# Kernel optimization log

Measured on AMD Instinct MI355X. Metric: run time of the kernel, lower is better.

The kernel has to match this reference:

```python
import jax, jax.numpy as jnp
import numpy as np

K = 3            # kernel size (odd)
CO, CI = 16, 16  # out/in channels

def setup_inputs() -> dict:
    key = jax.random.key(0)
    k1, k2, k3, k4 = jax.random.split(key, 4)
    B, C, H, W = 4, CI, 128, 128
    input_data = jax.random.normal(k1, (B, C, H, W), dtype=jnp.float32)
    # fixation coordinates in pixel units
    foa_xy = jax.random.uniform(k2, (B, 2), dtype=jnp.float32) * jnp.array([W, H], jnp.float32)
    hidden = 256
    W1 = jax.random.normal(k3, (2, hidden), dtype=jnp.float32) * (1.0 / jnp.sqrt(2.0))
    b1 = jnp.zeros((hidden,), jnp.float32)
    W2 = jax.random.normal(k4, (hidden, CO * CI * K * K), dtype=jnp.float32) * (1.0 / jnp.sqrt(hidden))
    b2 = jnp.zeros((CO * CI * K * K,), jnp.float32)
    return {"input_data": input_data, "foa_xy": foa_xy, "W1": W1, "b1": b1, "W2": W2, "b2": b2}

def _unfold_reflect(x, k):
    # x: [B, C, H, W] -> patches [B, C, k*k, H*W], reflect padding, stride 1, dilation 1
    B, C, H, W = x.shape
    pad = (k - 1) // 2
    xp = jnp.pad(x, ((0, 0), (0, 0), (pad, pad), (pad, pad)), mode="reflect")
    rows = [xp[:, :, i:i + H, j:j + W] for i in range(k) for j in range(k)]
    return jnp.stack(rows, axis=2).reshape(B, C, k * k, H * W)

def reference(input_data, foa_xy, W1, b1, W2, b2):
    B, C, H, W = input_data.shape
    # coordinate grid [H*W, 2] as (x, y), matching torch meshgrid(ij) + stack(xx, yy)
    ys = jnp.arange(H, dtype=jnp.float32)
    xs = jnp.arange(W, dtype=jnp.float32)
    yy, xx = jnp.meshgrid(ys, xs, indexing="ij")
    coords = jnp.stack([xx.ravel(), yy.ravel()], axis=1)         # [HW, 2]
    net_in = (coords[None, :, :] - foa_xy[:, None, :]).reshape(B * H * W, 2)
    # kernel-generating MLP
    h = jax.nn.relu(net_in @ W1 + b1)
    net_out = h @ W2 + b2                                        # [B*HW, CO*CI*K*K]
    kernel = net_out.reshape(B, H * W, CO, CI, K * K)            # [B, P, o, i, q]
    patches = _unfold_reflect(input_data, K)                     # [B, CI, K*K, HW]
    # per-pixel conv: sum over in-channels and kernel taps
    out = jnp.einsum("biqp,bpoiq->bop", patches, kernel)         # [B, CO, HW]
    return out.reshape(B, CO, H, W)
```

## Files before the change

kernel.cpp:

```cpp
#include <hip/hip_runtime.h>

#define CI    16
#define CO    16
#define HID   256
#define KPAD  288
#define NKK   9
#define NKH   8
#define NCH   144
#define IMGH  128
#define IMGW  128
#define NMS   8
#define RSTR  132
#define RLEN  130
#define KKSTR (NCH * 32)
#define OSTRS (NKK * NCH * 32)
#define MGOFF (4 * NKH * 512)

typedef float f32x4  __attribute__((ext_vector_type(4)));
typedef float f32x2  __attribute__((ext_vector_type(2)));
typedef short bf16x8 __attribute__((ext_vector_type(8)));

__device__ __host__ __forceinline__ short f2bf(float f) {
  union { float f; unsigned u; } c; c.f = f;
  unsigned b = c.u + 0x7FFFu + ((c.u >> 16) & 1u);
  return (short)(b >> 16);
}

__global__ void prep_w2(const float* __restrict__ W2, const float* __restrict__ b2,
                        short* __restrict__ W2b) {
  __shared__ float tile[32][65];
  const int kk = blockIdx.x % NKK;
  const int colbase = (blockIdx.x / NKK) * 64;
  const int tid = threadIdx.x;

  for (int e = tid; e < 2048; e += 256) {
    int klr = e >> 6;
    int cc  = e & 63;
    int col = colbase + cc;
    float v;
    if (kk < 8) v = W2[(kk * 32 + klr) * (CO * NCH) + col];
    else        v = (klr == 0) ? b2[col] : 0.f;
    tile[klr][cc] = v;
  }
  __syncthreads();
  for (int e = tid; e < 2048; e += 256) {
    int cc = e >> 5;
    int kl = e & 31;
    int col = colbase + cc;
    int o = col / NCH;
    int n = col - o * NCH;
    int i = n / 9, q = n - i * 9;
    int dyr = q / 3, dx = q - dyr * 3;
    int np = dx * 48 + i * 3 + dyr;
    W2b[(((o * NKK + kk) * NCH + np) << 5) + kl] = f2bf(tile[kl][cc]);
  }
}

__global__ __launch_bounds__(512, 4)
void ngconv_main(const float* __restrict__ in, const float* __restrict__ foa,
                 const float* __restrict__ W1, const float* __restrict__ b1,
                 const short* __restrict__ W2b, float* __restrict__ out) {
  __shared__ short shHf[64 * 512];
  __shared__ short shPatch[48 * RSTR];

  const int tid  = threadIdx.x;
  const int lane = tid & 63;
  const int wv8  = tid >> 6;
  const int mg   = wv8 >> 2;
  const int wo   = wv8 & 3;
  const int c15  = lane & 15;
  const int quad = lane >> 4;

  const int blk = blockIdx.x;
  const int b   = blk >> 7;
  const int y   = blk & 127;

  const float fx  = foa[b * 2 + 0];
  const float fy  = foa[b * 2 + 1];
  const float dyv = (float)y - fy;

  const int ry0 = (y == 0) ? 1 : (y - 1);
  const int ry2 = (y == IMGH - 1) ? (IMGH - 2) : (y + 1);

  for (int e = tid; e < 48 * RLEN; e += 512) {
    int r  = e / RLEN;
    int xx = e - r * RLEN;
    int i = r / 3, dyr = r - i * 3;
    int ryr = (dyr == 0) ? ry0 : ((dyr == 1) ? y : ry2);
    int x = xx - 1;
    x = (x < 0) ? 1 : ((x > IMGW - 1) ? (IMGW - 2) : x);
    shPatch[r * RSTR + xx] = f2bf(in[((b * CI + i) * IMGH + ryr) * IMGW + x]);
  }

  for (int g = tid; g < 128 * 32; g += 512) {
    int px = g & 127;
    int ks = g >> 7;
    int k0 = ks << 3;
    float dxv = (float)px - fx;
    short hv[8];
    #pragma unroll
    for (int j = 0; j < 8; ++j) {
      int k = k0 + j;
      float h = fmaxf(fmaf(dxv, W1[k], fmaf(dyv, W1[HID + k], b1[k])), 0.f);
      hv[j] = f2bf(h);
    }
    int ms = px >> 4;
    int kk = k0 >> 5;
    int lslot = ((k0 & 31) >> 3) * 16 + (px & 15);
    *(bf16x8*)&shHf[((ms * NKH + kk) << 9) + (lslot << 3)] = *(bf16x8*)hv;
  }

  bf16x8 af8 = (bf16x8){0, 0, 0, 0, 0, 0, 0, 0};
  if (quad == 0) af8[0] = (short)0x3F80;

  __syncthreads();

  const short* shHg = shHf + mg * MGOFF;

  #pragma unroll 1
  for (int oj = 0; oj < 4; ++oj) {
    const int o = wo + oj * 4;
    const short* Bo = W2b + o * OSTRS + (c15 << 5) + (quad << 3);

    f32x2 P2[8];
    #pragma unroll
    for (int t = 0; t < 8; ++t) P2[t] = (f32x2){0.f, 0.f};

    #pragma unroll 1
    for (int pass = 0; pass < 3; ++pass) {
      const short* Bp = Bo + (pass * 3) * 512;
      f32x4 acc[4][3];
      #pragma unroll
      for (int ms = 0; ms < 4; ++ms)
        #pragma unroll
        for (int j = 0; j < 3; ++j)
          acc[ms][j] = (f32x4){0.f, 0.f, 0.f, 0.f};

      bf16x8 bE[3], bO[3];
      #pragma unroll
      for (int j = 0; j < 3; ++j) bE[j] = *(const bf16x8*)&Bp[j << 9];

      #pragma unroll 1
      for (int t = 0; t < 4; ++t) {
        const int kkE = 2 * t;
        #pragma unroll
        for (int j = 0; j < 3; ++j)
          bO[j] = *(const bf16x8*)&Bp[(kkE + 1) * KKSTR + (j << 9)];
        {
          const short* hp = shHg + (kkE << 9) + (lane << 3);
          #pragma unroll
          for (int ms = 0; ms < 4; ++ms) {
            bf16x8 af = *(const bf16x8*)&hp[ms * (NKH << 9)];
            #pragma unroll
            for (int j = 0; j < 3; ++j)
              acc[ms][j] = __builtin_amdgcn_mfma_f32_16x16x32_bf16(
                  af, bE[j], acc[ms][j], 0, 0, 0);
          }
        }
        #pragma unroll
        for (int j = 0; j < 3; ++j)
          bE[j] = *(const bf16x8*)&Bp[(kkE + 2) * KKSTR + (j << 9)];
        {
          const short* hp = shHg + ((kkE + 1) << 9) + (lane << 3);
          #pragma unroll
          for (int ms = 0; ms < 4; ++ms) {
            bf16x8 af = *(const bf16x8*)&hp[ms * (NKH << 9)];
            #pragma unroll
            for (int j = 0; j < 3; ++j)
              acc[ms][j] = __builtin_amdgcn_mfma_f32_16x16x32_bf16(
                  af, bO[j], acc[ms][j], 0, 0, 0);
          }
        }
      }
      {
        #pragma unroll
        for (int ms = 0; ms < 4; ++ms)
          #pragma unroll
          for (int j = 0; j < 3; ++j)
            acc[ms][j] = __builtin_amdgcn_mfma_f32_16x16x32_bf16(
                af8, bE[j], acc[ms][j], 0, 0, 0);
      }

      const int sh = pass << 4;
      #pragma unroll
      for (int j = 0; j < 3; ++j) {
        const short* prow = &shPatch[((j << 4) + c15) * RSTR + (mg << 6) + (quad << 2)];
        #pragma unroll
        for (int ms = 0; ms < 4; ++ms) {
          uint2 u0 = *(const uint2*)&prow[ms * 16];
          unsigned u1 = *(const unsigned*)&prow[ms * 16 + 4];
          unsigned long long a0 =
              (unsigned long long)u0.x | ((unsigned long long)u0.y << 32);
          unsigned long long a1 =
              (unsigned long long)u0.y | ((unsigned long long)u1 << 32);
          unsigned d0 = (unsigned)(a0 >> sh);
          unsigned d1 = (unsigned)(a1 >> sh);
          float p0 = __uint_as_float(d0 << 16);
          float p1 = __uint_as_float(d0 & 0xFFFF0000u);
          float p2 = __uint_as_float(d1 << 16);
          float p3 = __uint_as_float(d1 & 0xFFFF0000u);
          f32x2 a01 = {acc[ms][j][0], acc[ms][j][1]};
          f32x2 a23 = {acc[ms][j][2], acc[ms][j][3]};
          P2[ms * 2 + 0] += a01 * (f32x2){p0, p1};
          P2[ms * 2 + 1] += a23 * (f32x2){p2, p3};
        }
      }
    }

    float P[16];
    #pragma unroll
    for (int t = 0; t < 16; ++t) P[t] = P2[t >> 1][t & 1];
    #pragma unroll
    for (int m = 8; m >= 1; m >>= 1) {
      const bool hi = (c15 & m) != 0;
      #pragma unroll
      for (int j = 0; j < m; ++j) {
        float keep = hi ? P[j + m] : P[j];
        float send = hi ? P[j] : P[j + m];
        float recv = __shfl_xor(send, m, 64);
        P[j] = keep + recv;
      }
    }

    const int x = (mg << 6) + (c15 >> 2) * 16 + quad * 4 + (c15 & 3);
    out[((b * CO + o) * IMGH + y) * IMGW + x] = P[0];
  }
}

extern "C" void kernel_launch(void* const* d_in, const int* in_sizes, int n_in,
                              void* d_out, int out_size, void* d_ws, size_t ws_size,
                              hipStream_t stream) {
  const float* in  = (const float*)d_in[0];
  const float* foa = (const float*)d_in[1];
  const float* W1  = (const float*)d_in[2];
  const float* b1  = (const float*)d_in[3];
  const float* W2  = (const float*)d_in[4];
  const float* b2  = (const float*)d_in[5];
  float* out = (float*)d_out;
  short* W2b = (short*)d_ws;

  prep_w2<<<324, 256, 0, stream>>>(W2, b2, W2b);
  ngconv_main<<<512, 512, 0, stream>>>(in, foa, W1, b1, W2b, out);
}
```

Baseline: 188.1 us.

## Halve block to 4 waves, compute two output channels per wave, stage stores in LDS

Shrinks the block from 8 to 4 waves. Each wave now accumulates two output channels at once, so every hidden-activation LDS fragment feeds twice as many MFMAs. Output rows are staged in shared memory and written as coalesced float2 stores instead of scattered per-lane stores. The cost is doubled accumulator registers (96 floats of acc plus 32 partial sums), fewer waves per block, and extra block-level barriers per channel pair.

```diff
diff --git a/kernel.cpp b/kernel.cpp
--- a/kernel.cpp
+++ b/kernel.cpp
@@ -9,7 +9,6 @@
 #define NCH   144
 #define IMGH  128
 #define IMGW  128
-#define NMS   8
 #define RSTR  132
 #define RLEN  130
 #define KKSTR (NCH * 32)
@@ -56,18 +55,19 @@
   }
 }
 
-__global__ __launch_bounds__(512, 4)
+__global__ __launch_bounds__(256, 2)
 void ngconv_main(const float* __restrict__ in, const float* __restrict__ foa,
                  const float* __restrict__ W1, const float* __restrict__ b1,
                  const short* __restrict__ W2b, float* __restrict__ out) {
   __shared__ short shHf[64 * 512];
   __shared__ short shPatch[48 * RSTR];
+  __shared__ float shOut[4 * IMGW];
 
   const int tid  = threadIdx.x;
   const int lane = tid & 63;
-  const int wv8  = tid >> 6;
-  const int mg   = wv8 >> 2;
-  const int wo   = wv8 & 3;
+  const int wv   = tid >> 6;
+  const int wo   = wv >> 1;
+  const int mg   = wv & 1;
   const int c15  = lane & 15;
   const int quad = lane >> 4;
 
@@ -82,7 +82,7 @@
   const int ry0 = (y == 0) ? 1 : (y - 1);
   const int ry2 = (y == IMGH - 1) ? (IMGH - 2) : (y + 1);
 
-  for (int e = tid; e < 48 * RLEN; e += 512) {
+  for (int e = tid; e < 48 * RLEN; e += 256) {
     int r  = e / RLEN;
     int xx = e - r * RLEN;
     int i = r / 3, dyr = r - i * 3;
@@ -92,7 +92,7 @@
     shPatch[r * RSTR + xx] = f2bf(in[((b * CI + i) * IMGH + ryr) * IMGW + x]);
   }
 
-  for (int g = tid; g < 128 * 32; g += 512) {
+  for (int g = tid; g < 128 * 32; g += 256) {
     int px = g & 127;
     int ks = g >> 7;
     int k0 = ks << 3;
@@ -118,67 +118,85 @@
   const short* shHg = shHf + mg * MGOFF;
 
   #pragma unroll 1
-  for (int oj = 0; oj < 4; ++oj) {
-    const int o = wo + oj * 4;
-    const short* Bo = W2b + o * OSTRS + (c15 << 5) + (quad << 3);
-
-    f32x2 P2[8];
+  for (int s = 0; s < 4; ++s) {
+    const int o0 = wo * 8 + 2 * s;
+    const short* Bo0 = W2b + o0 * OSTRS + (c15 << 5) + (quad << 3);
+
+    f32x2 P2[2][8];
     #pragma unroll
-    for (int t = 0; t < 8; ++t) P2[t] = (f32x2){0.f, 0.f};
+    for (int oi = 0; oi < 2; ++oi)
+      #pragma unroll
+      for (int t = 0; t < 8; ++t) P2[oi][t] = (f32x2){0.f, 0.f};
 
     #pragma unroll 1
     for (int pass = 0; pass < 3; ++pass) {
-      const short* Bp = Bo + (pass * 3) * 512;
-      f32x4 acc[4][3];
-      #pragma unroll
-      for (int ms = 0; ms < 4; ++ms)
-        #pragma unroll
-        for (int j = 0; j < 3; ++j)
-          acc[ms][j] = (f32x4){0.f, 0.f, 0.f, 0.f};
-
-      bf16x8 bE[3], bO[3];
-      #pragma unroll
-      for (int j = 0; j < 3; ++j) bE[j] = *(const bf16x8*)&Bp[j << 9];
+      const short* Bp0 = Bo0 + (pass * 3) * 512;
+      const short* Bp1 = Bp0 + OSTRS;
+      f32x4 acc[2][4][3];
+      #pragma unroll
+      for (int oi = 0; oi < 2; ++oi)
+        #pragma unroll
+        for (int ms = 0; ms < 4; ++ms)
+          #pragma unroll
+          for (int j = 0; j < 3; ++j)
+            acc[oi][ms][j] = (f32x4){0.f, 0.f, 0.f, 0.f};
+
+      bf16x8 bE[2][3], bO[2][3];
+      #pragma unroll
+      for (int j = 0; j < 3; ++j) {
+        bE[0][j] = *(const bf16x8*)&Bp0[j << 9];
+        bE[1][j] = *(const bf16x8*)&Bp1[j << 9];
+      }
 
       #pragma unroll 1
       for (int t = 0; t < 4; ++t) {
         const int kkE = 2 * t;
         #pragma unroll
-        for (int j = 0; j < 3; ++j)
-          bO[j] = *(const bf16x8*)&Bp[(kkE + 1) * KKSTR + (j << 9)];
+        for (int j = 0; j < 3; ++j) {
+          bO[0][j] = *(const bf16x8*)&Bp0[(kkE + 1) * KKSTR + (j << 9)];
+          bO[1][j] = *(const bf16x8*)&Bp1[(kkE + 1) * KKSTR + (j << 9)];
+        }
         {
           const short* hp = shHg + (kkE << 9) + (lane << 3);
           #pragma unroll
           for (int ms = 0; ms < 4; ++ms) {
             bf16x8 af = *(const bf16x8*)&hp[ms * (NKH << 9)];
             #pragma unroll
-            for (int j = 0; j < 3; ++j)
-              acc[ms][j] = __builtin_amdgcn_mfma_f32_16x16x32_bf16(
-                  af, bE[j], acc[ms][j], 0, 0, 0);
+            for (int oi = 0; oi < 2; ++oi)
+              #pragma unroll
+              for (int j = 0; j < 3; ++j)
+                acc[oi][ms][j] = __builtin_amdgcn_mfma_f32_16x16x32_bf16(
+                    af, bE[oi][j], acc[oi][ms][j], 0, 0, 0);
           }
         }
         #pragma unroll
-        for (int j = 0; j < 3; ++j)
-          bE[j] = *(const bf16x8*)&Bp[(kkE + 2) * KKSTR + (j << 9)];
+        for (int j = 0; j < 3; ++j) {
+          bE[0][j] = *(const bf16x8*)&Bp0[(kkE + 2) * KKSTR + (j << 9)];
+          bE[1][j] = *(const bf16x8*)&Bp1[(kkE + 2) * KKSTR + (j << 9)];
+        }
         {
           const short* hp = shHg + ((kkE + 1) << 9) + (lane << 3);
           #pragma unroll
           for (int ms = 0; ms < 4; ++ms) {
             bf16x8 af = *(const bf16x8*)&hp[ms * (NKH << 9)];
             #pragma unroll
+            for (int oi = 0; oi < 2; ++oi)
+              #pragma unroll
+              for (int j = 0; j < 3; ++j)
+                acc[oi][ms][j] = __builtin_amdgcn_mfma_f32_16x16x32_bf16(
+                    af, bO[oi][j], acc[oi][ms][j], 0, 0, 0);
+          }
+        }
+      }
+      {
+        #pragma unroll
+        for (int ms = 0; ms < 4; ++ms)
+          #pragma unroll
+          for (int oi = 0; oi < 2; ++oi)
+            #pragma unroll
             for (int j = 0; j < 3; ++j)
-              acc[ms][j] = __builtin_amdgcn_mfma_f32_16x16x32_bf16(
-                  af, bO[j], acc[ms][j], 0, 0, 0);
-          }
-        }
-      }
-      {
-        #pragma unroll
-        for (int ms = 0; ms < 4; ++ms)
-          #pragma unroll
-          for (int j = 0; j < 3; ++j)
-            acc[ms][j] = __builtin_amdgcn_mfma_f32_16x16x32_bf16(
-                af8, bE[j], acc[ms][j], 0, 0, 0);
+              acc[oi][ms][j] = __builtin_amdgcn_mfma_f32_16x16x32_bf16(
+                  af8, bE[oi][j], acc[oi][ms][j], 0, 0, 0);
       }
 
       const int sh = pass << 4;
@@ -199,31 +217,45 @@
           float p1 = __uint_as_float(d0 & 0xFFFF0000u);
           float p2 = __uint_as_float(d1 << 16);
           float p3 = __uint_as_float(d1 & 0xFFFF0000u);
-          f32x2 a01 = {acc[ms][j][0], acc[ms][j][1]};
-          f32x2 a23 = {acc[ms][j][2], acc[ms][j][3]};
-          P2[ms * 2 + 0] += a01 * (f32x2){p0, p1};
-          P2[ms * 2 + 1] += a23 * (f32x2){p2, p3};
-        }
-      }
-    }
-
-    float P[16];
+          #pragma unroll
+          for (int oi = 0; oi < 2; ++oi) {
+            f32x2 a01 = {acc[oi][ms][j][0], acc[oi][ms][j][1]};
+            f32x2 a23 = {acc[oi][ms][j][2], acc[oi][ms][j][3]};
+            P2[oi][ms * 2 + 0] += a01 * (f32x2){p0, p1};
+            P2[oi][ms * 2 + 1] += a23 * (f32x2){p2, p3};
+          }
+        }
+      }
+    }
+
     #pragma unroll
-    for (int t = 0; t < 16; ++t) P[t] = P2[t >> 1][t & 1];
-    #pragma unroll
-    for (int m = 8; m >= 1; m >>= 1) {
-      const bool hi = (c15 & m) != 0;
-      #pragma unroll
-      for (int j = 0; j < m; ++j) {
-        float keep = hi ? P[j + m] : P[j];
-        float send = hi ? P[j] : P[j + m];
-        float recv = __shfl_xor(send, m, 64);
-        P[j] = keep + recv;
-      }
-    }
-
-    const int x = (mg << 6) + (c15 >> 2) * 16 + quad * 4 + (c15 & 3);
-    out[((b * CO + o) * IMGH + y) * IMGW + x] = P[0];
+    for (int oi = 0; oi < 2; ++oi) {
+      float P[16];
+      #pragma unroll
+      for (int t = 0; t < 16; ++t) P[t] = P2[oi][t >> 1][t & 1];
+      #pragma unroll
+      for (int m = 8; m >= 1; m >>= 1) {
+        const bool hi = (c15 & m) != 0;
+        #pragma unroll
+        for (int j = 0; j < m; ++j) {
+          float keep = hi ? P[j + m] : P[j];
+          float send = hi ? P[j] : P[j + m];
+          float recv = __shfl_xor(send, m, 64);
+          P[j] = keep + recv;
+        }
+      }
+      const int px = (mg << 6) + (c15 >> 2) * 16 + quad * 4 + (c15 & 3);
+      shOut[(wo * 2 + oi) * IMGW + px] = P[0];
+    }
+    __syncthreads();
+    {
+      int r  = tid >> 6;
+      int c2 = tid & 63;
+      int o  = (r >> 1) * 8 + 2 * s + (r & 1);
+      float2 v = *(const float2*)&shOut[r * IMGW + c2 * 2];
+      *(float2*)&out[((b * CO + o) * IMGH + y) * IMGW + c2 * 2] = v;
+    }
+    __syncthreads();
   }
 }
 
@@ -240,5 +272,5 @@
   short* W2b = (short*)d_ws;
 
   prep_w2<<<324, 256, 0, stream>>>(W2, b2, W2b);
-  ngconv_main<<<512, 512, 0, stream>>>(in, foa, W1, b1, W2b, out);
-}
+  ngconv_main<<<512, 256, 0, stream>>>(in, foa, W1, b1, W2b, out);
+}
```

Result: faster. 158.6 us (-15.7%).
